# Kernel optimization log

Hardware: AMD Instinct MI355X
Metric: run time of the kernel (lower is better)

Reference implementation:

```python
import jax, jax.numpy as jnp
from jax import lax
import numpy as np


def setup_inputs() -> dict:
    key = jax.random.key(0)
    ks = jax.random.split(key, 7)
    B, T, I, H, O = 8192, 512, 7, 7, 1
    s = 1.0 / np.sqrt(H)
    return {
        "x": jax.random.normal(ks[0], (B, T, I), dtype=jnp.float32),
        "W_ih": jax.random.normal(ks[1], (H, I), dtype=jnp.float32) * s,
        "W_hh": jax.random.normal(ks[2], (H, H), dtype=jnp.float32) * s,
        "b_ih": jax.random.normal(ks[3], (H,), dtype=jnp.float32) * s,
        "b_hh": jax.random.normal(ks[4], (H,), dtype=jnp.float32) * s,
        "W_fc": jax.random.normal(ks[5], (O, H), dtype=jnp.float32) * s,
        "b_fc": jax.random.normal(ks[6], (O,), dtype=jnp.float32) * s,
    }


def reference(x, W_ih, W_hh, b_ih, b_hh, W_fc, b_fc):
    # Vanilla tanh RNN: h_t = tanh(x_t W_ih^T + b_ih + h_{t-1} W_hh^T + b_hh)
    B, T, _ = x.shape
    H = W_hh.shape[0]
    # Precompute the input projection for all timesteps (one big GEMM).
    xp = jnp.einsum("bti,hi->bth", x, W_ih) + (b_ih + b_hh)  # [B,T,H]
    h0 = jnp.zeros((B, H), dtype=x.dtype)

    def step(h, xt):
        h = jnp.tanh(xt + h @ W_hh.T)
        return h, h

    hT, hs = lax.scan(step, h0, jnp.swapaxes(xp, 0, 1))  # hs: [T,B,H]
    out_seq = jnp.swapaxes(hs, 0, 1)  # [B,T,H]
    out = (jnp.einsum("bth,oh->bto", out_seq, W_fc) + b_fc).squeeze(-1)  # [B,T]
    hidden = hT[None]  # [1,B,H] matching torch's (num_layers, B, H)
    return (out, hidden)
```

## Files before the change

### kernel.cpp

```cpp
#include <hip/hip_runtime.h>
#include <stdint.h>


#define B_TOTAL 8192
#define T_STEPS 512

#define DPP_QUAD0 0x00
#define DPP_QUAD1 0x55
#define DPP_QUAD2 0xAA
#define DPP_QUAD3 0xFF
#define DPP_XOR1  0xB1
#define DPP_XOR2  0x4E
#define DPP_HM    0x141

template <int CTRL>
__device__ __forceinline__ float dpp_mov(float v) {
    int s = __float_as_int(v);
    return __int_as_float(__builtin_amdgcn_update_dpp(s, s, CTRL, 0xF, 0xF, true));
}

typedef float v4f __attribute__((ext_vector_type(4)));

struct XChunk { v4f v[14]; };

__device__ __forceinline__ void chunk_issue(XChunk& ch, const float* base) {
    #pragma unroll
    for (int i = 0; i < 14; ++i)
        asm volatile("global_load_dwordx4 %0, %1, off offset:%2"
                     : "=v"(ch.v[i]) : "v"(base), "i"(16 * i));
}

#define CHUNK_WAIT(ch, N)                                                     \
    asm volatile("s_waitcnt vmcnt(" #N ")"                                    \
        : "+v"((ch).v[0]), "+v"((ch).v[1]), "+v"((ch).v[2]), "+v"((ch).v[3]), \
          "+v"((ch).v[4]), "+v"((ch).v[5]), "+v"((ch).v[6]), "+v"((ch).v[7]), \
          "+v"((ch).v[8]), "+v"((ch).v[9]), "+v"((ch).v[10]),                 \
          "+v"((ch).v[11]), "+v"((ch).v[12]), "+v"((ch).v[13]))

__global__ __launch_bounds__(256, 1) void rnn_kernel(
    const float* __restrict__ x,
    const float* __restrict__ Wih,
    const float* __restrict__ Whh,
    const float* __restrict__ bih,
    const float* __restrict__ bhh,
    const float* __restrict__ Wfc,
    const float* __restrict__ bfc,
    float* __restrict__ out)
{
    const int tid  = threadIdx.x;
    const int k    = tid & 7;
    const int b    = blockIdx.x * 32 + (tid >> 3);
    const int quad = (tid >> 2) & 1;

    const float C2L = 2.8853900817779268f;

    float wih[7];
    float wa[4], wb[4];
    float bias = 0.0f;
    float wfcm2 = 0.0f;
    float obase;
    {
        float whh_row[8];
        #pragma unroll
        for (int i = 0; i < 8; ++i) whh_row[i] = 0.0f;
        float wfc_own = 0.0f;
        if (k < 7) {
            float srow = 0.0f;
            #pragma unroll
            for (int i = 0; i < 7; ++i) {
                float wr = Whh[k * 7 + i];
                whh_row[i] = -2.0f * C2L * wr;
                srow += wr;
                wih[i] = C2L * Wih[k * 7 + i];
            }
            bias = C2L * (bih[k] + bhh[k] + srow);
            wfc_own = Wfc[k];
        } else {
            #pragma unroll
            for (int i = 0; i < 7; ++i) wih[i] = 0.0f;
        }
        wfcm2 = -2.0f * wfc_own;
        float ws = wfc_own;
        ws += dpp_mov<DPP_XOR1>(ws);
        ws += dpp_mov<DPP_XOR2>(ws);
        ws += dpp_mov<DPP_HM>(ws);
        obase = bfc[0] + ws;
        #pragma unroll
        for (int j = 0; j < 4; ++j) {
            wa[j] = quad ? whh_row[4 + j] : whh_row[j];
            wb[j] = quad ? whh_row[j]     : whh_row[4 + j];
        }
    }

    const float* xrow = x + (size_t)b * (T_STEPS * 7);
    float* outp = out + (size_t)b * T_STEPS;

    float a0 = 0.5f, a1 = 0.5f, a2 = 0.5f, a3 = 0.5f;
    float b0 = 0.5f, b1 = 0.5f, b2 = 0.5f, b3 = 0.5f;

    XChunk A, B;
    chunk_issue(A, xrow);
    chunk_issue(B, xrow + 56);

    auto do_chunk = [&](XChunk& buf, int c, const float* reload) {
        float u[8];
        {
            float xv[56];
            #pragma unroll
            for (int i = 0; i < 14; ++i) {
                xv[4 * i + 0] = buf.v[i].x; xv[4 * i + 1] = buf.v[i].y;
                xv[4 * i + 2] = buf.v[i].z; xv[4 * i + 3] = buf.v[i].w;
            }
            #pragma unroll
            for (int s = 0; s < 8; ++s) {
                const float* xs = &xv[s * 7];
                float p01 = __builtin_fmaf(wih[1], xs[1], wih[0] * xs[0]);
                float p23 = __builtin_fmaf(wih[3], xs[3], wih[2] * xs[2]);
                float p45 = __builtin_fmaf(wih[5], xs[5], wih[4] * xs[4]);
                float p6b = __builtin_fmaf(wih[6], xs[6], bias);
                u[s] = (p01 + p23) + (p45 + p6b);
            }
        }
        if (reload) chunk_issue(buf, reload);
        float rs[8];
        #pragma unroll
        for (int s = 0; s < 8; ++s) {
            float p0 = __builtin_fmaf(wa[0], a0, u[s]);
            float p1 = __builtin_fmaf(wa[2], a2, wa[1] * a1);
            float p2 = __builtin_fmaf(wb[0], b0, wa[3] * a3);
            float p3 = __builtin_fmaf(wb[2], b2, wb[1] * b1);
            float p4 = wb[3] * b3;
            float acc = (p0 + p1) + (p2 + (p3 + p4));
            float e  = __builtin_amdgcn_exp2f(acc);
            float rk = __builtin_amdgcn_rcpf(e + 1.0f);
            rs[s] = rk;
            a0 = dpp_mov<DPP_QUAD0>(rk);
            a1 = dpp_mov<DPP_QUAD1>(rk);
            a2 = dpp_mov<DPP_QUAD2>(rk);
            a3 = dpp_mov<DPP_QUAD3>(rk);
            b0 = dpp_mov<DPP_HM>(a0);
            b1 = dpp_mov<DPP_HM>(a1);
            b2 = dpp_mov<DPP_HM>(a2);
            b3 = dpp_mov<DPP_HM>(a3);
        }
        float o[8];
        #pragma unroll
        for (int s = 0; s < 8; ++s) {
            float v = wfcm2 * rs[s];
            v += dpp_mov<DPP_XOR1>(v);
            v += dpp_mov<DPP_XOR2>(v);
            v += dpp_mov<DPP_HM>(v);
            o[s] = v + obase;
        }
        if (k == 7) {
            *(float4*)(outp + c * 8 + 0) = make_float4(o[0], o[1], o[2], o[3]);
            *(float4*)(outp + c * 8 + 4) = make_float4(o[4], o[5], o[6], o[7]);
        }
    };

    #pragma unroll 1
    for (int c = 0; c < 62; c += 2) {
        CHUNK_WAIT(A, 14);
        do_chunk(A, c, xrow + (c + 2) * 56);
        CHUNK_WAIT(B, 14);
        do_chunk(B, c + 1, xrow + (c + 3) * 56);
    }
    CHUNK_WAIT(A, 14);
    do_chunk(A, 62, nullptr);
    CHUNK_WAIT(B, 0);
    do_chunk(B, 63, nullptr);

    if (k < 7) {
        int kk = k & 3;
        float rv = (kk == 0) ? a0 : (kk == 1) ? a1 : (kk == 2) ? a2 : a3;
        out[(size_t)B_TOTAL * T_STEPS + (size_t)b * 7 + k] =
            __builtin_fmaf(-2.0f, rv, 1.0f);
    }
}

extern "C" void kernel_launch(void* const* d_in, const int* in_sizes, int n_in,
                              void* d_out, int out_size, void* d_ws, size_t ws_size,
                              hipStream_t stream) {
    const float* x   = (const float*)d_in[0];
    const float* Wih = (const float*)d_in[1];
    const float* Whh = (const float*)d_in[2];
    const float* bih = (const float*)d_in[3];
    const float* bhh = (const float*)d_in[4];
    const float* Wfc = (const float*)d_in[5];
    const float* bfc = (const float*)d_in[6];
    float* out = (float*)d_out;

    rnn_kernel<<<dim3(B_TOTAL / 32), dim3(256), 0, stream>>>(
        x, Wih, Whh, bih, bhh, Wfc, bfc, out);
}
```

Baseline: 208.0 us.

## Split each hidden unit's recurrent dot product across 16 lanes per batch row

```diff
diff --git a/kernel.cpp b/kernel.cpp
--- a/kernel.cpp
+++ b/kernel.cpp
@@ -5,13 +5,14 @@
 #define B_TOTAL 8192
 #define T_STEPS 512
 
-#define DPP_QUAD0 0x00
-#define DPP_QUAD1 0x55
-#define DPP_QUAD2 0xAA
-#define DPP_QUAD3 0xFF
-#define DPP_XOR1  0xB1
-#define DPP_XOR2  0x4E
-#define DPP_HM    0x141
+#define DPP_Q0   0x00
+#define DPP_Q1   0x55
+#define DPP_Q2   0xAA
+#define DPP_Q3   0xFF
+#define DPP_XOR1 0xB1
+#define DPP_XOR2 0x4E
+#define DPP_ROR4 0x124
+#define DPP_ROR8 0x128
 
 template <int CTRL>
 __device__ __forceinline__ float dpp_mov(float v) {
@@ -37,7 +38,7 @@
           "+v"((ch).v[8]), "+v"((ch).v[9]), "+v"((ch).v[10]),                 \
           "+v"((ch).v[11]), "+v"((ch).v[12]), "+v"((ch).v[13]))
 
-__global__ __launch_bounds__(256, 1) void rnn_kernel(
+__global__ __launch_bounds__(256, 2) void rnn_kernel(
     const float* __restrict__ x,
     const float* __restrict__ Wih,
     const float* __restrict__ Whh,
@@ -48,55 +49,60 @@
     float* __restrict__ out)
 {
     const int tid  = threadIdx.x;
-    const int k    = tid & 7;
-    const int b    = blockIdx.x * 32 + (tid >> 3);
-    const int quad = (tid >> 2) & 1;
+    const int lane = tid & 63;
+    const int p    = lane & 15;
+    const int q    = p >> 2;
+    const int j    = p & 3;
+    const int row  = ((q & 1) << 2) | j;
+    const bool lowq = (q < 2);
+    const int b    = blockIdx.x * 16 + (tid >> 4);
 
     const float C2L = 2.8853900817779268f;
 
-    float wih[7];
-    float wa[4], wb[4];
-    float bias = 0.0f;
-    float wfcm2 = 0.0f;
+    float wu[7];
+    #pragma unroll
+    for (int i = 0; i < 7; ++i) wu[i] = 0.0f;
+    float useed = 0.0f, wfch = 0.0f;
+    float wd[4] = {0.f, 0.f, 0.f, 0.f}, we[4] = {0.f, 0.f, 0.f, 0.f};
     float obase;
     {
-        float whh_row[8];
+        float Wp[8];
         #pragma unroll
-        for (int i = 0; i < 8; ++i) whh_row[i] = 0.0f;
-        float wfc_own = 0.0f;
-        if (k < 7) {
+        for (int i = 0; i < 8; ++i) Wp[i] = 0.0f;
+        if (row < 7) {
             float srow = 0.0f;
             #pragma unroll
-            for (int i = 0; i < 7; ++i) {
-                float wr = Whh[k * 7 + i];
-                whh_row[i] = -2.0f * C2L * wr;
+            for (int c = 0; c < 7; ++c) {
+                float wr = Whh[row * 7 + c];
+                Wp[c] = -2.0f * C2L * wr;
                 srow += wr;
-                wih[i] = C2L * Wih[k * 7 + i];
             }
-            bias = C2L * (bih[k] + bhh[k] + srow);
-            wfc_own = Wfc[k];
-        } else {
-            #pragma unroll
-            for (int i = 0; i < 7; ++i) wih[i] = 0.0f;
+            if (lowq) {
+                #pragma unroll
+                for (int c = 0; c < 4; ++c) wu[c] = C2L * Wih[row * 7 + c];
+                useed = C2L * (bih[row] + bhh[row] + srow);
+            } else {
+                #pragma unroll
+                for (int c = 4; c < 7; ++c) wu[c] = C2L * Wih[row * 7 + c];
+            }
+            wfch = -Wfc[row];
         }
-        wfcm2 = -2.0f * wfc_own;
-        float ws = wfc_own;
-        ws += dpp_mov<DPP_XOR1>(ws);
-        ws += dpp_mov<DPP_XOR2>(ws);
-        ws += dpp_mov<DPP_HM>(ws);
-        obase = bfc[0] + ws;
         #pragma unroll
-        for (int j = 0; j < 4; ++j) {
-            wa[j] = quad ? whh_row[4 + j] : whh_row[j];
-            wb[j] = quad ? whh_row[j]     : whh_row[4 + j];
+        for (int jj = 0; jj < 4; ++jj) {
+            float lo = Wp[jj], hi = Wp[4 + jj];
+            wd[jj] = (q == 0) ? lo : (q == 3) ? hi : 0.0f;
+            we[jj] = (q == 1) ? lo : (q == 2) ? hi : 0.0f;
         }
+        float sw = 0.0f;
+        #pragma unroll
+        for (int r7 = 0; r7 < 7; ++r7) sw += Wfc[r7];
+        obase = bfc[0] + sw;
     }
 
     const float* xrow = x + (size_t)b * (T_STEPS * 7);
     float* outp = out + (size_t)b * T_STEPS;
 
-    float a0 = 0.5f, a1 = 0.5f, a2 = 0.5f, a3 = 0.5f;
-    float b0 = 0.5f, b1 = 0.5f, b2 = 0.5f, b3 = 0.5f;
+    float rk = 0.5f;
 
     XChunk A, B;
     chunk_issue(A, xrow);
@@ -114,45 +120,39 @@
             #pragma unroll
             for (int s = 0; s < 8; ++s) {
                 const float* xs = &xv[s * 7];
-                float p01 = __builtin_fmaf(wih[1], xs[1], wih[0] * xs[0]);
-                float p23 = __builtin_fmaf(wih[3], xs[3], wih[2] * xs[2]);
-                float p45 = __builtin_fmaf(wih[5], xs[5], wih[4] * xs[4]);
-                float p6b = __builtin_fmaf(wih[6], xs[6], bias);
-                u[s] = (p01 + p23) + (p45 + p6b);
+                float acc = useed;
+                #pragma unroll
+                for (int c7 = 0; c7 < 7; ++c7)
+                    acc = __builtin_fmaf(wu[c7], xs[c7], acc);
+                u[s] = acc;
             }
         }
         if (reload) chunk_issue(buf, reload);
-        float rs[8];
-        #pragma unroll
-        for (int s = 0; s < 8; ++s) {
-            float p0 = __builtin_fmaf(wa[0], a0, u[s]);
-            float p1 = __builtin_fmaf(wa[2], a2, wa[1] * a1);
-            float p2 = __builtin_fmaf(wb[0], b0, wa[3] * a3);
-            float p3 = __builtin_fmaf(wb[2], b2, wb[1] * b1);
-            float p4 = wb[3] * b3;
-            float acc = (p0 + p1) + (p2 + (p3 + p4));
-            float e  = __builtin_amdgcn_exp2f(acc);
-            float rk = __builtin_amdgcn_rcpf(e + 1.0f);
-            rs[s] = rk;
-            a0 = dpp_mov<DPP_QUAD0>(rk);
-            a1 = dpp_mov<DPP_QUAD1>(rk);
-            a2 = dpp_mov<DPP_QUAD2>(rk);
-            a3 = dpp_mov<DPP_QUAD3>(rk);
-            b0 = dpp_mov<DPP_HM>(a0);
-            b1 = dpp_mov<DPP_HM>(a1);
-            b2 = dpp_mov<DPP_HM>(a2);
-            b3 = dpp_mov<DPP_HM>(a3);
-        }
+
         float o[8];
         #pragma unroll
         for (int s = 0; s < 8; ++s) {
-            float v = wfcm2 * rs[s];
+            float d0 = dpp_mov<DPP_Q0>(rk), d1 = dpp_mov<DPP_Q1>(rk);
+            float d2 = dpp_mov<DPP_Q2>(rk), d3 = dpp_mov<DPP_Q3>(rk);
+            float e0 = dpp_mov<DPP_ROR4>(d0), e1 = dpp_mov<DPP_ROR4>(d1);
+            float e2 = dpp_mov<DPP_ROR4>(d2), e3 = dpp_mov<DPP_ROR4>(d3);
+            float aa = __builtin_fmaf(wd[0], d0, u[s]);
+            aa = __builtin_fmaf(wd[1], d1, aa);
+            float bb = wd[2] * d2; bb = __builtin_fmaf(wd[3], d3, bb);
+            float cc = we[0] * e0; cc = __builtin_fmaf(we[1], e1, cc);
+            float gg = we[2] * e2; gg = __builtin_fmaf(we[3], e3, gg);
+            float acc = (aa + bb) + (cc + gg);
+            acc += dpp_mov<DPP_ROR8>(acc);
+            float ee = __builtin_amdgcn_exp2f(acc);
+            rk = __builtin_amdgcn_rcpf(ee + 1.0f);
+            float v = wfch * rk;
             v += dpp_mov<DPP_XOR1>(v);
             v += dpp_mov<DPP_XOR2>(v);
-            v += dpp_mov<DPP_HM>(v);
+            v += dpp_mov<DPP_ROR4>(v);
+            v += dpp_mov<DPP_ROR8>(v);
             o[s] = v + obase;
         }
-        if (k == 7) {
+        if (p == 15) {
             *(float4*)(outp + c * 8 + 0) = make_float4(o[0], o[1], o[2], o[3]);
             *(float4*)(outp + c * 8 + 4) = make_float4(o[4], o[5], o[6], o[7]);
         }
@@ -170,11 +170,9 @@
     CHUNK_WAIT(B, 0);
     do_chunk(B, 63, nullptr);
 
-    if (k < 7) {
-        int kk = k & 3;
-        float rv = (kk == 0) ? a0 : (kk == 1) ? a1 : (kk == 2) ? a2 : a3;
-        out[(size_t)B_TOTAL * T_STEPS + (size_t)b * 7 + k] =
-            __builtin_fmaf(-2.0f, rv, 1.0f);
+    if (p < 8 && row < 7) {
+        out[(size_t)B_TOTAL * T_STEPS + (size_t)b * 7 + row] =
+            __builtin_fmaf(-2.0f, rk, 1.0f);
     }
 }
 
@@ -190,6 +188,6 @@
     const float* bfc = (const float*)d_in[6];
     float* out = (float*)d_out;
 
-    rnn_kernel<<<dim3(B_TOTAL / 32), dim3(256), 0, stream>>>(
+    rnn_kernel<<<dim3(B_TOTAL / 16), dim3(256), 0, stream>>>(
         x, Wih, Whh, bih, bhh, Wfc, bfc, out);
 }
```

Measured after the change: 242.1 us. 16.4% more time.
